# Performance work log

Measured on AMD Instinct MI355X. Metric: run time of the kernel, lower is better.

Reference implementation:

```python
import jax, jax.numpy as jnp
import numpy as np

N_CLASS = 8192
FEAT_DIM = 1024
BATCH = 1024
PROTO_M = 0.95
TEMP = 0.1
BASE_TEMP = 0.1
EPS = 1e-12  # F.normalize eps


def setup_inputs() -> dict:
    key = jax.random.key(0)
    k1, k2, k3 = jax.random.split(key, 3)
    features = jax.random.normal(k1, (BATCH, FEAT_DIM), dtype=jnp.float32)
    labels = jax.random.randint(k2, (BATCH,), 0, N_CLASS)
    prototypes = jax.random.normal(k3, (N_CLASS, FEAT_DIM), dtype=jnp.float32)
    # init_class_prototypes ends with F.normalize(prototypes, dim=1)
    prototypes = prototypes / jnp.maximum(
        jnp.linalg.norm(prototypes, axis=1, keepdims=True), EPS)
    return {"features": features, "labels": labels, "prototypes": prototypes}


def _ema_update(prototypes, features, labels):
    # Sequential per-sample EMA scatter update (order matters for repeated labels),
    # expressed as a lax.scan over the batch.
    def step(protos, fl):
        f, l = fl
        row = protos[l] * PROTO_M + f * (1.0 - PROTO_M)
        row = row / jnp.maximum(jnp.linalg.norm(row), EPS)  # F.normalize(dim=0)
        return protos.at[l].set(row), None

    protos, _ = jax.lax.scan(step, prototypes, (features, labels))
    return protos


def reference(features, labels, prototypes):
    protos = _ema_update(prototypes, features, labels)  # [C, D]
    logits = jnp.matmul(protos, protos.T) / TEMP        # [C, C]
    exp_l = jnp.exp(logits)
    # mask = off-diagonal ones (labels are arange(n_class)), so the masked sum
    # is the row sum minus the diagonal; mask.sum(1) == n_class - 1 (never NaN).
    sum_neg = exp_l.sum(axis=1) - jnp.diagonal(exp_l)   # [C]
    mean_prob_neg = jnp.log(sum_neg / jnp.float32(N_CLASS - 1))
    loss = (TEMP / BASE_TEMP) * jnp.mean(mean_prob_neg)
    return loss
```

## Files before the change

kernel.cpp:

```cpp
#include <hip/hip_runtime.h>
#include <math.h>

#define C 8192
#define D 1024
#define BATCH 1024
#define PM 0.95f
#define PMC 0.05f
#define INVT_SCALED 0.15625f

typedef unsigned char u8;
typedef __attribute__((ext_vector_type(16))) float f32x16;

#define GLOBAL_AS(p) ((const __attribute__((address_space(1))) void*)(p))
#define LDS_AS(p) ((__attribute__((address_space(3))) void*)(p))

__global__ __launch_bounds__(256) void ema_split_kernel(const float* __restrict__ feat,
                                                        const int* __restrict__ labels,
                                                        const float* __restrict__ protos,
                                                        u8* __restrict__ P8,
                                                        float* __restrict__ rowsum,
                                                        float* __restrict__ out) {
    __shared__ int sl[BATCH];
    const int t = threadIdx.x, w = t >> 6, lane = t & 63;
    const int c = blockIdx.x * 4 + w;

    if (blockIdx.x < 32) rowsum[blockIdx.x * 256 + t] = 0.0f;
    if (blockIdx.x == 0 && t == 0) out[0] = 0.0f;

    for (int i = t; i < BATCH; i += 256) sl[i] = labels[i];
    __syncthreads();

    float4 v[4];
    #pragma unroll
    for (int s = 0; s < 4; ++s)
        v[s] = *(const float4*)(protos + (size_t)c * D + s * 256 + lane * 4);

    for (int base = 0; base < BATCH; base += 64) {
        unsigned long long mask = __ballot(sl[base + lane] == c);
        while (mask) {
            const int b = __ffsll((long long)mask) - 1;
            mask &= mask - 1;
            const int idx = base + b;
            float ss = 0.0f;
            #pragma unroll
            for (int s = 0; s < 4; ++s) {
                const float4 f = *(const float4*)(feat + (size_t)idx * D + s * 256 + lane * 4);
                v[s].x = v[s].x * PM + f.x * PMC;
                v[s].y = v[s].y * PM + f.y * PMC;
                v[s].z = v[s].z * PM + f.z * PMC;
                v[s].w = v[s].w * PM + f.w * PMC;
                ss += v[s].x * v[s].x + v[s].y * v[s].y + v[s].z * v[s].z + v[s].w * v[s].w;
            }
            #pragma unroll
            for (int off = 32; off > 0; off >>= 1) ss += __shfl_xor(ss, off);
            const float inv = 1.0f / fmaxf(sqrtf(ss), 1e-12f);
            #pragma unroll
            for (int s = 0; s < 4; ++s) {
                v[s].x *= inv; v[s].y *= inv; v[s].z *= inv; v[s].w *= inv;
            }
        }
    }

    u8* ob = P8 + (size_t)(c >> 5) * 32768 + (c & 31) * 8;
    #pragma unroll
    for (int s = 0; s < 4; ++s) {
        const int k0 = s * 256 + lane * 4;
        const size_t off = (size_t)(k0 >> 4) * 512 + ((k0 >> 3) & 1) * 256 + (k0 & 7);
        int p = __builtin_amdgcn_cvt_pk_fp8_f32(v[s].x * 8.0f, v[s].y * 8.0f, 0, false);
        p = __builtin_amdgcn_cvt_pk_fp8_f32(v[s].z * 8.0f, v[s].w * 8.0f, p, true);
        *(unsigned int*)(ob + off) = (unsigned int)p;
    }
}

__global__ __launch_bounds__(256, 4) void gram8_kernel(const u8* __restrict__ P8,
                                                       float* __restrict__ rowsum) {
    __shared__ u8 lds[2][16384];
    __shared__ float rpart[128];
    __shared__ float cpart[128];
    const int t = threadIdx.x, w = t >> 6, lane = t & 63;

    int mm = blockIdx.x >> 3;
    const int r = blockIdx.x & 7;
    int bi = 0;
    #pragma unroll
    for (int s = 0; s < 8; ++s) {
        const int strip = (s & 1) ? ((s >> 1) * 16 + 15 - r) : ((s >> 1) * 16 + r);
        const int n = 64 - strip;
        if (mm < n) { bi = strip; break; }
        mm -= n;
    }
    const int bj = bi + mm;
    const bool diag = (bi == bj);

    if (t < 128) { rpart[t] = 0.0f; cpart[t] = 0.0f; }

    const u8* gsrc[4];
    int ldst[4];
    #pragma unroll
    for (int gg = 0; gg < 4; ++gg) {
        const int g = gg * 4 + w;
        const int region = g >> 3;
        const int a = (g & 7) >> 1, p = g & 1;
        const int RT = (region ? bj : bi) * 4 + a;
        gsrc[gg] = P8 + (size_t)RT * 32768 + p * 1024 + lane * 16;
        ldst[gg] = region * 8192 + a * 2048 + p * 1024;
    }

    const int qi = w >> 1, qj = w & 1;
    f32x16 acc[2][2];
    #pragma unroll
    for (int a = 0; a < 2; ++a)
        #pragma unroll
        for (int b = 0; b < 2; ++b)
            #pragma unroll
            for (int e = 0; e < 16; ++e) acc[a][b][e] = 0.0f;

    #pragma unroll
    for (int gg = 0; gg < 4; ++gg)
        __builtin_amdgcn_global_load_lds(GLOBAL_AS(gsrc[gg]),
                                         LDS_AS(&lds[0][ldst[gg]]), 16, 0, 0);

    for (int kc = 0; kc < 16; ++kc) {
        const int cur = kc & 1;
        __syncthreads();
        if (kc < 15) {
            #pragma unroll
            for (int gg = 0; gg < 4; ++gg)
                __builtin_amdgcn_global_load_lds(GLOBAL_AS(gsrc[gg] + (size_t)(kc + 1) * 2048),
                                                 LDS_AS(&lds[cur ^ 1][ldst[gg]]), 16, 0, 0);
        }
        #pragma unroll
        for (int kk = 0; kk < 4; ++kk) {
            long af[2], bf[2];
            #pragma unroll
            for (int ti = 0; ti < 2; ++ti)
                af[ti] = *(const long*)&lds[cur][((qi * 2 + ti) * 4 + kk) * 512 + lane * 8];
            #pragma unroll
            for (int tj = 0; tj < 2; ++tj)
                bf[tj] = *(const long*)&lds[cur][8192 + ((qj * 2 + tj) * 4 + kk) * 512 + lane * 8];
            #pragma unroll
            for (int ti = 0; ti < 2; ++ti)
                #pragma unroll
                for (int tj = 0; tj < 2; ++tj)
                    acc[ti][tj] = __builtin_amdgcn_mfma_f32_32x32x16_fp8_fp8(
                        af[ti], bf[tj], acc[ti][tj], 0, 0, 0);
        }
    }

    __syncthreads();
    const int half = lane >> 5, col = lane & 31;
    float csum[2] = {0.0f, 0.0f};
    #pragma unroll
    for (int ti = 0; ti < 2; ++ti) {
        float rs[16];
        #pragma unroll
        for (int reg = 0; reg < 16; ++reg) rs[reg] = 0.0f;
        #pragma unroll
        for (int tj = 0; tj < 2; ++tj) {
            const int lj = qj * 64 + tj * 32 + col;
            #pragma unroll
            for (int reg = 0; reg < 16; ++reg) {
                const int li = qi * 64 + ti * 32 + (reg & 3) + 8 * (reg >> 2) + 4 * half;
                float e = __expf(acc[ti][tj][reg] * INVT_SCALED);
                if (diag && li >= lj) e = 0.0f;
                rs[reg] += e;
                csum[tj] += e;
            }
        }
        #pragma unroll
        for (int reg = 0; reg < 16; ++reg) {
            float v = rs[reg];
            v += __shfl_xor(v, 1); v += __shfl_xor(v, 2); v += __shfl_xor(v, 4);
            v += __shfl_xor(v, 8); v += __shfl_xor(v, 16);
            if (col == 0)
                atomicAdd(&rpart[qi * 64 + ti * 32 + (reg & 3) + 8 * (reg >> 2) + 4 * half], v);
        }
    }
    #pragma unroll
    for (int tj = 0; tj < 2; ++tj) {
        float v = csum[tj];
        v += __shfl_xor(v, 32);
        if (half == 0) atomicAdd(&cpart[qj * 64 + tj * 32 + col], v);
    }
    __syncthreads();
    if (t < 128) atomicAdd(&rowsum[bi * 128 + t], rpart[t]);
    else         atomicAdd(&rowsum[bj * 128 + (t - 128)], cpart[t - 128]);
}

__global__ __launch_bounds__(256) void final2_kernel(const float* __restrict__ rowsum,
                                                     float* __restrict__ out) {
    __shared__ float red[4];
    const int t = threadIdx.x;
    const int i = blockIdx.x * 256 + t;
    float v = logf(rowsum[i] * (1.0f / (float)(C - 1)));
    #pragma unroll
    for (int off = 32; off > 0; off >>= 1) v += __shfl_down(v, off);
    if ((t & 63) == 0) red[t >> 6] = v;
    __syncthreads();
    if (t == 0)
        atomicAdd(out, (red[0] + red[1] + red[2] + red[3]) * (1.0f / (float)C));
}

extern "C" void kernel_launch(void* const* d_in, const int* in_sizes, int n_in,
                              void* d_out, int out_size, void* d_ws, size_t ws_size,
                              hipStream_t stream) {
    const float* feat = (const float*)d_in[0];
    const int* labels = (const int*)d_in[1];
    const float* protos = (const float*)d_in[2];
    float* out = (float*)d_out;
    float* rowsum = (float*)d_ws;
    u8* P8 = (u8*)((char*)d_ws + 32768);

    ema_split_kernel<<<C / 4, 256, 0, stream>>>(feat, labels, protos, P8, rowsum, out);
    gram8_kernel<<<2080, 256, 0, stream>>>(P8, rowsum);
    final2_kernel<<<C / 256, 256, 0, stream>>>(rowsum, out);
}
```

Measured before the change: 153.3 us.

## Switch Gram kernel to 32x32x64 scaled FP8 MFMA with matching operand layout

Replaces the four 32x32x16 fp8 MFMAs per K-chunk with a single gfx950 mfma_scale 32x32x64 f8f6f4 instruction, using unit scales (0x7F exponent). The prototype-packing layout written by the EMA kernel is changed so each lane reads two contiguous 16-byte LDS chunks forming the 32-byte operand. This is meant to cut MFMA issue count and LDS load instructions by using the wider-K instruction, at the risk of an operand-layout mismatch giving wrong results.

```diff
diff --git a/kernel.cpp b/kernel.cpp
--- a/kernel.cpp
+++ b/kernel.cpp
@@ -9,6 +9,8 @@
 #define INVT_SCALED 0.15625f
 
 typedef unsigned char u8;
+typedef __attribute__((ext_vector_type(4))) int i32x4;
+typedef __attribute__((ext_vector_type(8))) int i32x8;
 typedef __attribute__((ext_vector_type(16))) float f32x16;
 
 #define GLOBAL_AS(p) ((const __attribute__((address_space(1))) void*)(p))
@@ -61,11 +63,13 @@
         }
     }
 
-    u8* ob = P8 + (size_t)(c >> 5) * 32768 + (c & 31) * 8;
+    const int rt = c >> 5, r = c & 31;
+    u8* ob = P8 + (size_t)rt * 32768;
     #pragma unroll
     for (int s = 0; s < 4; ++s) {
         const int k0 = s * 256 + lane * 4;
-        const size_t off = (size_t)(k0 >> 4) * 512 + ((k0 >> 3) & 1) * 256 + (k0 & 7);
+        const size_t off = (size_t)(k0 >> 6) * 2048 + ((k0 >> 4) & 1) * 1024
+                         + (r + 32 * ((k0 >> 5) & 1)) * 16 + (k0 & 15);
         int p = __builtin_amdgcn_cvt_pk_fp8_f32(v[s].x * 8.0f, v[s].y * 8.0f, 0, false);
         p = __builtin_amdgcn_cvt_pk_fp8_f32(v[s].z * 8.0f, v[s].w * 8.0f, p, true);
         *(unsigned int*)(ob + off) = (unsigned int)p;
@@ -129,22 +133,28 @@
                 __builtin_amdgcn_global_load_lds(GLOBAL_AS(gsrc[gg] + (size_t)(kc + 1) * 2048),
                                                  LDS_AS(&lds[cur ^ 1][ldst[gg]]), 16, 0, 0);
         }
-        #pragma unroll
-        for (int kk = 0; kk < 4; ++kk) {
-            long af[2], bf[2];
-            #pragma unroll
-            for (int ti = 0; ti < 2; ++ti)
-                af[ti] = *(const long*)&lds[cur][((qi * 2 + ti) * 4 + kk) * 512 + lane * 8];
+        i32x8 af[2], bf[2];
+        #pragma unroll
+        for (int ti = 0; ti < 2; ++ti) {
+            const int a = qi * 2 + ti;
+            const i32x4 lo = *(const i32x4*)&lds[cur][a * 2048 + lane * 16];
+            const i32x4 hi = *(const i32x4*)&lds[cur][a * 2048 + 1024 + lane * 16];
+            af[ti] = __builtin_shufflevector(lo, hi, 0, 1, 2, 3, 4, 5, 6, 7);
+        }
+        #pragma unroll
+        for (int tj = 0; tj < 2; ++tj) {
+            const int b = qj * 2 + tj;
+            const i32x4 lo = *(const i32x4*)&lds[cur][8192 + b * 2048 + lane * 16];
+            const i32x4 hi = *(const i32x4*)&lds[cur][8192 + b * 2048 + 1024 + lane * 16];
+            bf[tj] = __builtin_shufflevector(lo, hi, 0, 1, 2, 3, 4, 5, 6, 7);
+        }
+        #pragma unroll
+        for (int ti = 0; ti < 2; ++ti)
             #pragma unroll
             for (int tj = 0; tj < 2; ++tj)
-                bf[tj] = *(const long*)&lds[cur][8192 + ((qj * 2 + tj) * 4 + kk) * 512 + lane * 8];
-            #pragma unroll
-            for (int ti = 0; ti < 2; ++ti)
-                #pragma unroll
-                for (int tj = 0; tj < 2; ++tj)
-                    acc[ti][tj] = __builtin_amdgcn_mfma_f32_32x32x16_fp8_fp8(
-                        af[ti], bf[tj], acc[ti][tj], 0, 0, 0);
-        }
+                acc[ti][tj] = __builtin_amdgcn_mfma_scale_f32_32x32x64_f8f6f4(
+                    af[ti], bf[tj], acc[ti][tj], 0, 0,
+                    0, 0x7F7F7F7F, 0, 0x7F7F7F7F);
     }
 
     __syncthreads();
```

Measured after the change: 432.4 us. 182% more time.

## Triple-buffer gram kernel LDS with smaller K-chunks and explicit vmcnt waits

Applied to the files above, without the earlier changes.

Replaces the double-buffered 2KB-per-tile K-chunk pipeline in the FP8 Gram kernel with a three-stage ring of 1KB chunks, issuing loads two chunks ahead. The waits become an explicit s_waitcnt vmcnt(2) plus a raw s_barrier instead of __syncthreads. The goal is to overlap global-to-LDS transfers with MFMA work while keeping the LDS footprint near its previous size. The cost is twice as many barriers per tile and a hand-managed wait count, which must stay correct for the loads to be complete before they are read.

```diff
diff --git a/kernel.cpp b/kernel.cpp
--- a/kernel.cpp
+++ b/kernel.cpp
@@ -74,7 +74,7 @@
 
 __global__ __launch_bounds__(256, 4) void gram8_kernel(const u8* __restrict__ P8,
                                                        float* __restrict__ rowsum) {
-    __shared__ u8 lds[2][16384];
+    __shared__ u8 lds[3][8192];
     __shared__ float rpart[128];
     __shared__ float cpart[128];
     const int t = threadIdx.x, w = t >> 6, lane = t & 63;
@@ -94,17 +94,9 @@
 
     if (t < 128) { rpart[t] = 0.0f; cpart[t] = 0.0f; }
 
-    const u8* gsrc[4];
-    int ldst[4];
-    #pragma unroll
-    for (int gg = 0; gg < 4; ++gg) {
-        const int g = gg * 4 + w;
-        const int region = g >> 3;
-        const int a = (g & 7) >> 1, p = g & 1;
-        const int RT = (region ? bj : bi) * 4 + a;
-        gsrc[gg] = P8 + (size_t)RT * 32768 + p * 1024 + lane * 16;
-        ldst[gg] = region * 8192 + a * 2048 + p * 1024;
-    }
+    const u8* gsrcA = P8 + (size_t)(bi * 4 + w) * 32768 + lane * 16;
+    const u8* gsrcB = P8 + (size_t)(bj * 4 + w) * 32768 + lane * 16;
+    const int ldsA = w * 1024, ldsB = 4096 + w * 1024;
 
     const int qi = w >> 1, qj = w & 1;
     f32x16 acc[2][2];
@@ -115,29 +107,30 @@
             #pragma unroll
             for (int e = 0; e < 16; ++e) acc[a][b][e] = 0.0f;
 
-    #pragma unroll
-    for (int gg = 0; gg < 4; ++gg)
-        __builtin_amdgcn_global_load_lds(GLOBAL_AS(gsrc[gg]),
-                                         LDS_AS(&lds[0][ldst[gg]]), 16, 0, 0);
-
-    for (int kc = 0; kc < 16; ++kc) {
-        const int cur = kc & 1;
-        __syncthreads();
-        if (kc < 15) {
-            #pragma unroll
-            for (int gg = 0; gg < 4; ++gg)
-                __builtin_amdgcn_global_load_lds(GLOBAL_AS(gsrc[gg] + (size_t)(kc + 1) * 2048),
-                                                 LDS_AS(&lds[cur ^ 1][ldst[gg]]), 16, 0, 0);
-        }
-        #pragma unroll
-        for (int kk = 0; kk < 4; ++kk) {
+    __builtin_amdgcn_global_load_lds(GLOBAL_AS(gsrcA), LDS_AS(&lds[0][ldsA]), 16, 0, 0);
+    __builtin_amdgcn_global_load_lds(GLOBAL_AS(gsrcB), LDS_AS(&lds[0][ldsB]), 16, 0, 0);
+    __builtin_amdgcn_global_load_lds(GLOBAL_AS(gsrcA + 1024), LDS_AS(&lds[1][ldsA]), 16, 0, 0);
+    __builtin_amdgcn_global_load_lds(GLOBAL_AS(gsrcB + 1024), LDS_AS(&lds[1][ldsB]), 16, 0, 0);
+
+    int cb = 0, sb = 2;
+    for (int kc = 0; kc < 31; ++kc) {
+        asm volatile("s_waitcnt vmcnt(2)" ::: "memory");
+        __builtin_amdgcn_s_barrier();
+        if (kc < 30) {
+            __builtin_amdgcn_global_load_lds(GLOBAL_AS(gsrcA + (size_t)(kc + 2) * 1024),
+                                             LDS_AS(&lds[sb][ldsA]), 16, 0, 0);
+            __builtin_amdgcn_global_load_lds(GLOBAL_AS(gsrcB + (size_t)(kc + 2) * 1024),
+                                             LDS_AS(&lds[sb][ldsB]), 16, 0, 0);
+        }
+        #pragma unroll
+        for (int kk = 0; kk < 2; ++kk) {
             long af[2], bf[2];
             #pragma unroll
             for (int ti = 0; ti < 2; ++ti)
-                af[ti] = *(const long*)&lds[cur][((qi * 2 + ti) * 4 + kk) * 512 + lane * 8];
+                af[ti] = *(const long*)&lds[cb][(qi * 2 + ti) * 1024 + kk * 512 + lane * 8];
             #pragma unroll
             for (int tj = 0; tj < 2; ++tj)
-                bf[tj] = *(const long*)&lds[cur][8192 + ((qj * 2 + tj) * 4 + kk) * 512 + lane * 8];
+                bf[tj] = *(const long*)&lds[cb][4096 + (qj * 2 + tj) * 1024 + kk * 512 + lane * 8];
             #pragma unroll
             for (int ti = 0; ti < 2; ++ti)
                 #pragma unroll
@@ -145,6 +138,26 @@
                     acc[ti][tj] = __builtin_amdgcn_mfma_f32_32x32x16_fp8_fp8(
                         af[ti], bf[tj], acc[ti][tj], 0, 0, 0);
         }
+        cb = (cb == 2) ? 0 : cb + 1;
+        sb = (sb == 2) ? 0 : sb + 1;
+    }
+    asm volatile("s_waitcnt vmcnt(0)" ::: "memory");
+    __builtin_amdgcn_s_barrier();
+    #pragma unroll
+    for (int kk = 0; kk < 2; ++kk) {
+        long af[2], bf[2];
+        #pragma unroll
+        for (int ti = 0; ti < 2; ++ti)
+            af[ti] = *(const long*)&lds[cb][(qi * 2 + ti) * 1024 + kk * 512 + lane * 8];
+        #pragma unroll
+        for (int tj = 0; tj < 2; ++tj)
+            bf[tj] = *(const long*)&lds[cb][4096 + (qj * 2 + tj) * 1024 + kk * 512 + lane * 8];
+        #pragma unroll
+        for (int ti = 0; ti < 2; ++ti)
+            #pragma unroll
+            for (int tj = 0; tj < 2; ++tj)
+                acc[ti][tj] = __builtin_amdgcn_mfma_f32_32x32x16_fp8_fp8(
+                    af[ti], bf[tj], acc[ti][tj], 0, 0, 0);
     }
 
     __syncthreads();
```

New measurement: 163.0 us. +6.4%, slower.

## Give each wave a private LDS double buffer and drop block barriers in gram loop

Applied to the files above, without the earlier changes.

Each wave now loads its own A and B fragments into a private LDS double buffer and waits with s_waitcnt vmcnt instead of block-wide __syncthreads, so waves in the main K loop no longer synchronise with each other. Chunks shrink to 1 KB per tile and the loop runs 32 fully unrolled steps. The cost is that each tile is fetched redundantly by the two waves that share it, which doubles global and L2 traffic, and the rpart/cpart scratch now reuses the LDS buffer.

```diff
diff --git a/kernel.cpp b/kernel.cpp
--- a/kernel.cpp
+++ b/kernel.cpp
@@ -74,9 +74,7 @@
 
 __global__ __launch_bounds__(256, 4) void gram8_kernel(const u8* __restrict__ P8,
                                                        float* __restrict__ rowsum) {
-    __shared__ u8 lds[2][16384];
-    __shared__ float rpart[128];
-    __shared__ float cpart[128];
+    __shared__ u8 lds[4][2][4096];
     const int t = threadIdx.x, w = t >> 6, lane = t & 63;
 
     int mm = blockIdx.x >> 3;
@@ -92,61 +90,60 @@
     const int bj = bi + mm;
     const bool diag = (bi == bj);
 
+    const int qi = w >> 1, qj = w & 1;
+    const u8* gs[4];
+    gs[0] = P8 + (size_t)(bi * 4 + qi * 2 + 0) * 32768 + lane * 16;
+    gs[1] = P8 + (size_t)(bi * 4 + qi * 2 + 1) * 32768 + lane * 16;
+    gs[2] = P8 + (size_t)(bj * 4 + qj * 2 + 0) * 32768 + lane * 16;
+    gs[3] = P8 + (size_t)(bj * 4 + qj * 2 + 1) * 32768 + lane * 16;
+    u8* lb = &lds[w][0][0];
+
+    f32x16 acc[2][2];
+    #pragma unroll
+    for (int a = 0; a < 2; ++a)
+        #pragma unroll
+        for (int b = 0; b < 2; ++b)
+            #pragma unroll
+            for (int e = 0; e < 16; ++e) acc[a][b][e] = 0.0f;
+
+#define WAITV(N) asm volatile("s_waitcnt vmcnt(" #N ")" ::: "memory")
+
+    #pragma unroll
+    for (int u = 0; u < 4; ++u)
+        __builtin_amdgcn_global_load_lds(GLOBAL_AS(gs[u]),
+                                         LDS_AS(lb + u * 1024), 16, 0, 0);
+    #pragma unroll
+    for (int u = 0; u < 4; ++u)
+        __builtin_amdgcn_global_load_lds(GLOBAL_AS(gs[u] + 1024),
+                                         LDS_AS(lb + 4096 + u * 1024), 16, 0, 0);
+
+    #pragma unroll
+    for (int kc = 0; kc < 32; ++kc) {
+        if (kc < 31) { WAITV(4); } else { WAITV(0); }
+        const int bufo = (kc & 1) * 4096;
+        #pragma unroll
+        for (int kk = 0; kk < 2; ++kk) {
+            long a0 = *(const long*)(lb + bufo + 0 * 1024 + kk * 512 + lane * 8);
+            long a1 = *(const long*)(lb + bufo + 1 * 1024 + kk * 512 + lane * 8);
+            long b0 = *(const long*)(lb + bufo + 2 * 1024 + kk * 512 + lane * 8);
+            long b1 = *(const long*)(lb + bufo + 3 * 1024 + kk * 512 + lane * 8);
+            acc[0][0] = __builtin_amdgcn_mfma_f32_32x32x16_fp8_fp8(a0, b0, acc[0][0], 0, 0, 0);
+            acc[0][1] = __builtin_amdgcn_mfma_f32_32x32x16_fp8_fp8(a0, b1, acc[0][1], 0, 0, 0);
+            acc[1][0] = __builtin_amdgcn_mfma_f32_32x32x16_fp8_fp8(a1, b0, acc[1][0], 0, 0, 0);
+            acc[1][1] = __builtin_amdgcn_mfma_f32_32x32x16_fp8_fp8(a1, b1, acc[1][1], 0, 0, 0);
+        }
+        if (kc < 30) {
+            #pragma unroll
+            for (int u = 0; u < 4; ++u)
+                __builtin_amdgcn_global_load_lds(GLOBAL_AS(gs[u] + (size_t)(kc + 2) * 1024),
+                                                 LDS_AS(lb + bufo + u * 1024), 16, 0, 0);
+        }
+    }
+
+    __syncthreads();
+    float* rpart = (float*)&lds[0][0][0];
+    float* cpart = (float*)&lds[0][0][512];
     if (t < 128) { rpart[t] = 0.0f; cpart[t] = 0.0f; }
-
-    const u8* gsrc[4];
-    int ldst[4];
-    #pragma unroll
-    for (int gg = 0; gg < 4; ++gg) {
-        const int g = gg * 4 + w;
-        const int region = g >> 3;
-        const int a = (g & 7) >> 1, p = g & 1;
-        const int RT = (region ? bj : bi) * 4 + a;
-        gsrc[gg] = P8 + (size_t)RT * 32768 + p * 1024 + lane * 16;
-        ldst[gg] = region * 8192 + a * 2048 + p * 1024;
-    }
-
-    const int qi = w >> 1, qj = w & 1;
-    f32x16 acc[2][2];
-    #pragma unroll
-    for (int a = 0; a < 2; ++a)
-        #pragma unroll
-        for (int b = 0; b < 2; ++b)
-            #pragma unroll
-            for (int e = 0; e < 16; ++e) acc[a][b][e] = 0.0f;
-
-    #pragma unroll
-    for (int gg = 0; gg < 4; ++gg)
-        __builtin_amdgcn_global_load_lds(GLOBAL_AS(gsrc[gg]),
-                                         LDS_AS(&lds[0][ldst[gg]]), 16, 0, 0);
-
-    for (int kc = 0; kc < 16; ++kc) {
-        const int cur = kc & 1;
-        __syncthreads();
-        if (kc < 15) {
-            #pragma unroll
-            for (int gg = 0; gg < 4; ++gg)
-                __builtin_amdgcn_global_load_lds(GLOBAL_AS(gsrc[gg] + (size_t)(kc + 1) * 2048),
-                                                 LDS_AS(&lds[cur ^ 1][ldst[gg]]), 16, 0, 0);
-        }
-        #pragma unroll
-        for (int kk = 0; kk < 4; ++kk) {
-            long af[2], bf[2];
-            #pragma unroll
-            for (int ti = 0; ti < 2; ++ti)
-                af[ti] = *(const long*)&lds[cur][((qi * 2 + ti) * 4 + kk) * 512 + lane * 8];
-            #pragma unroll
-            for (int tj = 0; tj < 2; ++tj)
-                bf[tj] = *(const long*)&lds[cur][8192 + ((qj * 2 + tj) * 4 + kk) * 512 + lane * 8];
-            #pragma unroll
-            for (int ti = 0; ti < 2; ++ti)
-                #pragma unroll
-                for (int tj = 0; tj < 2; ++tj)
-                    acc[ti][tj] = __builtin_amdgcn_mfma_f32_32x32x16_fp8_fp8(
-                        af[ti], bf[tj], acc[ti][tj], 0, 0, 0);
-        }
-    }
-
     __syncthreads();
     const int half = lane >> 5, col = lane & 31;
     float csum[2] = {0.0f, 0.0f};
```

Result: slower. 163.7 us (+6.8%).
